# Kernel optimization log

Measured on AMD Instinct MI355X. Metric: run time of the kernel, lower is better.

The kernel has to match this reference:

```python
import jax, jax.numpy as jnp
import numpy as np

D = 1024

def setup_inputs() -> dict:
    key = jax.random.key(0)
    ks = jax.random.split(key, 9)
    B, S = 4, 2048
    s = 1.0 / np.sqrt(D)
    return {
        "query": jax.random.normal(ks[0], (B, S, D), jnp.float32),
        "key": jax.random.normal(ks[1], (B, S, D), jnp.float32),
        "value": jax.random.normal(ks[2], (B, S, D), jnp.float32),
        "Wq": jax.random.normal(ks[3], (D, D), jnp.float32) * s,
        "bq": jax.random.normal(ks[4], (D,), jnp.float32) * 0.01,
        "Wk": jax.random.normal(ks[5], (D, D), jnp.float32) * s,
        "bk": jax.random.normal(ks[6], (D,), jnp.float32) * 0.01,
        "Wv": jax.random.normal(ks[7], (D, D), jnp.float32) * s,
        "bv": jax.random.normal(ks[8], (D,), jnp.float32) * 0.01,
    }

def reference(query, key, value, Wq, bq, Wk, bk, Wv, bv):
    scale = 1.0 / (query.shape[-1] ** 0.5)
    q = jnp.einsum('bsd,ed->bse', query, Wq) + bq  # nn.Linear: x @ W.T + b
    k = jnp.einsum('bsd,ed->bse', key, Wk) + bk
    v = jnp.einsum('bsd,ed->bse', value, Wv) + bv
    scores = jnp.einsum('bqd,bkd->bqk', q, k) * scale  # [B, Sq, Skv]
    w = jax.nn.softmax(scores, axis=-1)
    return jnp.einsum('bqk,bkd->bqd', w, v)
```

## Files before the change

### kernel.cpp

```cpp
#include <hip/hip_runtime.h>

typedef __bf16 bf16x8 __attribute__((ext_vector_type(8)));
typedef float f32x4 __attribute__((ext_vector_type(4)));
typedef unsigned short u16x8 __attribute__((ext_vector_type(8)));

__device__ inline unsigned short f2bf(float f) {
  union { float f; unsigned u; } a; a.f = f;
  return (unsigned short)((a.u + 0x7fffu + ((a.u >> 16) & 1u)) >> 16);
}
__device__ inline float bf2f(unsigned short h) {
  union { unsigned u; float f; } a; a.u = ((unsigned)h) << 16;
  return a.f;
}

__global__ __launch_bounds__(256) void cvtW(const float* __restrict__ Wq,
                                            const float* __restrict__ Wk,
                                            const float* __restrict__ Wv,
                                            unsigned short* __restrict__ Wb) {
  int i = blockIdx.x * 256 + threadIdx.x;
  int idx = i >> 18;
  int off = i & 262143;
  const float* s = (idx == 0) ? Wq : ((idx == 1) ? Wk : Wv);
  float4 v = ((const float4*)s)[off];
  ushort4 o;
  o.x = f2bf(v.x); o.y = f2bf(v.y); o.z = f2bf(v.z); o.w = f2bf(v.w);
  ((ushort4*)(Wb + idx * 1048576))[off] = o;
}

#define G2L(gp, lp) __builtin_amdgcn_global_load_lds( \
    (const __attribute__((address_space(1))) void*)(gp), \
    (__attribute__((address_space(3))) void*)(lp), 16, 0, 0)

#define MFMA_(d, a, b) d = __builtin_amdgcn_mfma_f32_16x16x32_bf16(a, b, d, 0, 0, 0)
#define SB0() __builtin_amdgcn_sched_barrier(0)
#define LGKM(n) do { asm volatile("s_waitcnt lgkmcnt(" #n ")" ::: "memory"); SB0(); } while (0)
#define VMC(n) do { asm volatile("s_waitcnt vmcnt(" #n ")" ::: "memory"); SB0(); } while (0)

struct PJ {
  const float* A0; const float* A1; const float* A2;
  const unsigned short* B;
  unsigned short* outQ; unsigned short* outK; unsigned short* outV;
  const float* biasQ; const float* biasK; const float* biasV;
};

__global__ __launch_bounds__(256) void gemmP(PJ p) {
  extern __shared__ char smem[];
  char* smA = smem;
  char* smB = smem + 32768;
  const int tid = threadIdx.x, lane = tid & 63, wid = tid >> 6;
  const int wm = wid >> 1, wn = wid & 1;

  int orig = blockIdx.x + 8 * (blockIdx.y + 64 * blockIdx.z);
  int wg = (orig & 7) * 192 + (orig >> 3);
  int bx = wg & 7; int t2 = wg >> 3; int by = t2 & 63; int z = t2 >> 6;
  const int m0 = by << 7, n0 = bx << 7;

  const float* Az = (z == 0) ? p.A0 : ((z == 1) ? p.A1 : p.A2);

  const char* srcA0 = (const char*)Az + ((long long)m0 + (tid >> 4)) * 4096
                    + ((tid & 15) << 4);
  const int trow = tid >> 3;
  const int cs = (((tid & 7) ^ (trow & 7)) << 4);
  const char* srcB = (const char*)(p.B + (long long)z * 1048576
                                   + (long long)(n0 + trow) * 1024) + cs;

  const int aRowB = (((wm << 6) + (lane & 15)) << 7);
  const int bRowB = (((wn << 6) + (lane & 15)) << 7);
  const int csw = (lane & 7) << 4;
  const int ck0 = (((lane >> 4) << 4)) ^ csw;
  const int ck1 = ((((lane >> 4) << 4)) | 64) ^ csw;

  f32x4 acc[4][4];
#pragma unroll
  for (int i = 0; i < 4; ++i)
#pragma unroll
    for (int j = 0; j < 4; ++j) acc[i][j] = (f32x4){0.f, 0.f, 0.f, 0.f};

  float4 aregA[8], aregB[8];
  bf16x8 aLo[2][2], aHi[2][2], bLo[2][2], bHi[2][2];

  auto ldA = [&](int t, float4 (&ar)[8]) {
    const char* s = srcA0 + (long long)t * 256;
#pragma unroll
    for (int c = 0; c < 8; ++c)
      ar[c] = *(const float4*)(s + (long long)c * 65536);
  };
  auto wrA = [&](int t, float4 (&ar)[8]) {
    char* dA = smA + ((t & 1) << 14);
    const int g = (tid & 15) >> 1;
    const int hb = (tid & 1) << 3;
#pragma unroll
    for (int c = 0; c < 8; ++c) {
      const int rc = (c << 4) + (tid >> 4);
      float4 v = ar[c];
      union { __bf16 b[4]; ushort4 u; } o;
      o.b[0] = (__bf16)v.x; o.b[1] = (__bf16)v.y;
      o.b[2] = (__bf16)v.z; o.b[3] = (__bf16)v.w;
      *(ushort4*)(dA + (rc << 7) + ((g ^ (rc & 7)) << 4) + hb) = o.u;
    }
  };
  auto stageB = [&](int t, int b) {
    char* dB = smB + (b << 14) + (tid << 4);
    const char* sB = srcB + (long long)t * 128;
#pragma unroll
    for (int c = 0; c < 4; ++c)
      G2L(sB + (long long)c * 65536, dB + (c << 12));
  };
  auto readAh = [&](int b, int half, bf16x8 (&dst)[2][2]) {
    const char* ra = smA + (b << 14) + aRowB + (half << 12);
#pragma unroll
    for (int mi = 0; mi < 2; ++mi) {
      dst[mi][0] = *(const bf16x8*)(ra + (mi << 11) + ck0);
      dst[mi][1] = *(const bf16x8*)(ra + (mi << 11) + ck1);
    }
  };
  auto readBh = [&](int b, int half, bf16x8 (&dst)[2][2]) {
    const char* rb = smB + (b << 14) + bRowB + (half << 12);
#pragma unroll
    for (int ni = 0; ni < 2; ++ni) {
      dst[ni][0] = *(const bf16x8*)(rb + (ni << 11) + ck0);
      dst[ni][1] = *(const bf16x8*)(rb + (ni << 11) + ck1);
    }
  };
  auto quad = [&](int qa, int qb, bf16x8 (&A)[2][2], bf16x8 (&B)[2][2]) {
    __builtin_amdgcn_s_setprio(1);
#pragma unroll
    for (int mi = 0; mi < 2; ++mi)
#pragma unroll
      for (int ni = 0; ni < 2; ++ni) {
        MFMA_(acc[qa * 2 + mi][qb * 2 + ni], A[mi][0], B[ni][0]);
        MFMA_(acc[qa * 2 + mi][qb * 2 + ni], A[mi][1], B[ni][1]);
      }
    __builtin_amdgcn_s_setprio(0);
  };

  const int NT = 16;
  int b0 = 0, b1 = 1, b2 = 2;

  ldA(0, aregA); stageB(0, 0);
  ldA(1, aregB); stageB(1, 1);
  VMC(12);
  wrA(0, aregA);
  LGKM(0);
  __builtin_amdgcn_s_barrier();
  readAh(0, 0, aLo); readBh(0, 0, bLo);
  SB0();

  auto body = [&](int t, float4 (&arW)[8], float4 (&arL)[8]) {
    const bool pf1 = (t + 1) < NT, pf2 = (t + 2) < NT;
    if (pf2) { ldA(t + 2, arL); stageB(t + 2, b2); }
    readAh(t & 1, 1, aHi);
    SB0();
    LGKM(4);
    quad(0, 0, aLo, bLo);
    readBh(b0, 1, bHi);
    SB0();
    LGKM(4);
    quad(1, 0, aHi, bLo);
    LGKM(0);
    quad(0, 1, aLo, bHi);
    quad(1, 1, aHi, bHi);
    if (pf2) { VMC(12); }
    else     { VMC(0);  }
    if (pf1) wrA(t + 1, arW);
    LGKM(0);
    __builtin_amdgcn_s_barrier();
    if (pf1) { readAh((t + 1) & 1, 0, aLo); readBh(b1, 0, bLo); }
    SB0();
    int tmp = b0; b0 = b1; b1 = b2; b2 = tmp;
  };
  for (int t = 0; t < NT; t += 2) { body(t, aregB, aregA); body(t + 1, aregA, aregB); }

  const int c0 = lane & 15, r0 = (lane >> 4) << 2;
  if (z < 2) {
    unsigned short* O = (z == 0) ? p.outQ : p.outK;
    const float* bias = (z == 0) ? p.biasQ : p.biasK;
#pragma unroll
    for (int mi = 0; mi < 4; ++mi) {
      const int grow = m0 + (wm << 6) + (mi << 4) + r0;
#pragma unroll
      for (int ni = 0; ni < 4; ++ni) {
        const int gcol = n0 + (wn << 6) + (ni << 4) + c0;
        const float bb = bias[gcol];
#pragma unroll
        for (int rr = 0; rr < 4; ++rr)
          O[(long long)(grow + rr) * 1024 + gcol] = f2bf(acc[mi][ni][rr] + bb);
      }
    }
  } else {
#pragma unroll
    for (int mi = 0; mi < 4; ++mi) {
      const int grow = m0 + (wm << 6) + (mi << 4) + r0;
      const int bb = grow >> 11, s = grow & 2047;
#pragma unroll
      for (int ni = 0; ni < 4; ++ni) {
        const int d = n0 + (wn << 6) + (ni << 4) + c0;
        const float ba = p.biasV[d];
        ushort4 pk;
        pk.x = f2bf(acc[mi][ni][0] + ba);
        pk.y = f2bf(acc[mi][ni][1] + ba);
        pk.z = f2bf(acc[mi][ni][2] + ba);
        pk.w = f2bf(acc[mi][ni][3] + ba);
        *(ushort4*)(p.outV + ((long long)bb << 21) + (long long)d * 2048 + s) = pk;
      }
    }
  }
}

#define EPI_SCALE 1
#define EPI_OUT 2

struct GP {
  const unsigned short* A;
  const unsigned short* B;
  unsigned short* C;
  long long batchA, batchB, batchC;
  int lda, ldb, ldc, K;
  float scale;
};

template<int BM, int BN, int WMW, int WNW, int EPI>
__global__ __launch_bounds__(512, 2) void gemm2(GP p) {
  constexpr int NWN = BN / WNW;
  constexpr int AMF = WMW / 16, BNF = WNW / 16;
  constexpr int AH = AMF / 2, BH = BNF / 2;
  constexpr int AF_N = AH * 2;
  constexpr int NBA = BM / 64, NBB = BN / 64;
  static_assert((BM / WMW) * NWN == 8, "8 waves");
  static_assert(BNF == 4, "lgkm immediates assume BNF==4");

  extern __shared__ char smem[];
  char* smA = smem;
  char* smB = smem + 2 * BM * 128;

  const int tid = threadIdx.x;
  const int lane = tid & 63;
  const int wid = tid >> 6;
  const int wm = wid / NWN, wn = wid % NWN;

  const int gx = gridDim.x, gy = gridDim.y;
  const int nwg = gx * gy * (int)gridDim.z;
  int orig = blockIdx.x + gx * (blockIdx.y + gy * blockIdx.z);
  int qq = nwg >> 3, rr_ = nwg & 7;
  int xcd = orig & 7, sl = orig >> 3;
  int wg = (xcd < rr_ ? xcd * (qq + 1) : rr_ * (qq + 1) + (xcd - rr_) * qq) + sl;
  int bx = wg % gx;
  int t2 = wg / gx;
  int by = t2 % gy;
  int z  = t2 / gy;

  const int m0 = by * BM, n0 = bx * BN;

  const long long lda2 = (long long)p.lda * 2;
  const long long ldb2 = (long long)p.ldb * 2;
  const char* Abase = (const char*)(p.A + (long long)z * p.batchA) + (long long)m0 * lda2;
  const char* Bbase = (const char*)(p.B + (long long)z * p.batchB) + (long long)n0 * ldb2;

  const int trow = tid >> 3;
  const int cs = (((tid & 7) ^ (trow & 7)) << 4);
  const char* srcA = Abase + (long long)trow * lda2 + cs;
  const char* srcB = Bbase + (long long)trow * ldb2 + cs;

  const int NT = p.K >> 6;

  const int aRowB = ((wm * WMW + (lane & 15)) << 7);
  const int bRowB = ((wn * WNW + (lane & 15)) << 7);
  const int csw = (lane & 7) << 4;
  const int ck0 = (((lane >> 4) << 4)) ^ csw;
  const int ck1 = ((((lane >> 4) << 4)) | 64) ^ csw;

  f32x4 acc[AMF][BNF];
#pragma unroll
  for (int i = 0; i < AMF; ++i)
#pragma unroll
    for (int j = 0; j < BNF; ++j) acc[i][j] = (f32x4){0.f, 0.f, 0.f, 0.f};

  bf16x8 aLo[AH][2], aHi[AH][2], bLo[BH][2], bHi[BH][2];

  auto stage = [&](int t) {
    char* dA = smA + (t & 1) * (BM * 128) + (tid << 4);
    char* dB = smB + (t & 1) * (BN * 128) + (tid << 4);
    const char* sA = srcA + (long long)t * 128;
    const char* sB = srcB + (long long)t * 128;
#pragma unroll
    for (int c = 0; c < NBA; ++c) G2L(sA + (long long)c * (lda2 << 6), dA + c * 8192);
#pragma unroll
    for (int c = 0; c < NBB; ++c) G2L(sB + (long long)c * (ldb2 << 6), dB + c * 8192);
  };
  auto readAh = [&](int t, int half, bf16x8 (&dst)[AH][2]) {
    const char* ra = smA + (t & 1) * (BM * 128) + aRowB + half * (AH * 2048);
#pragma unroll
    for (int mi = 0; mi < AH; ++mi) {
      dst[mi][0] = *(const bf16x8*)(ra + mi * 2048 + ck0);
      dst[mi][1] = *(const bf16x8*)(ra + mi * 2048 + ck1);
    }
  };
  auto readBh = [&](int t, int half, bf16x8 (&dst)[BH][2]) {
    const char* rb = smB + (t & 1) * (BN * 128) + bRowB + half * (BH * 2048);
#pragma unroll
    for (int ni = 0; ni < BH; ++ni) {
      dst[ni][0] = *(const bf16x8*)(rb + ni * 2048 + ck0);
      dst[ni][1] = *(const bf16x8*)(rb + ni * 2048 + ck1);
    }
  };
  auto quad = [&](int qa, int qb, bf16x8 (&A)[AH][2], bf16x8 (&B)[BH][2]) {
    __builtin_amdgcn_s_setprio(1);
#pragma unroll
    for (int mi = 0; mi < AH; ++mi)
#pragma unroll
      for (int ni = 0; ni < BH; ++ni) {
        MFMA_(acc[qa * AH + mi][qb * BH + ni], A[mi][0], B[ni][0]);
        MFMA_(acc[qa * AH + mi][qb * BH + ni], A[mi][1], B[ni][1]);
      }
    __builtin_amdgcn_s_setprio(0);
  };

  stage(0); stage(1);
  if constexpr (NBA + NBB == 8) VMC(8); else VMC(6);
  __builtin_amdgcn_s_barrier();
  readAh(0, 0, aLo); readBh(0, 0, bLo);
  SB0();

  for (int t = 0; t < NT; ++t) {
    readAh(t, 1, aHi);
    SB0();
    if constexpr (AF_N == 8) LGKM(8); else LGKM(4);
    quad(0, 0, aLo, bLo);
    readBh(t, 1, bHi);
    SB0();
    LGKM(4);
    quad(1, 0, aHi, bLo);
    LGKM(0);
    quad(0, 1, aLo, bHi);
    quad(1, 1, aHi, bHi);
    VMC(0);
    __builtin_amdgcn_s_barrier();
    if (t + 2 < NT) stage(t + 2);
    if (t + 1 < NT) { readAh(t + 1, 0, aLo); readBh(t + 1, 0, bLo); }
    SB0();
  }

  const int c0 = lane & 15;
  const int r0 = (lane >> 4) << 2;
  if constexpr (EPI == EPI_SCALE) {
    unsigned short* Cz = p.C + (long long)z * p.batchC;
#pragma unroll
    for (int mi = 0; mi < AMF; ++mi) {
      const int grow = m0 + wm * WMW + (mi << 4) + r0;
#pragma unroll
      for (int ni = 0; ni < BNF; ++ni) {
        const int gcol = n0 + wn * WNW + (ni << 4) + c0;
#pragma unroll
        for (int rr = 0; rr < 4; ++rr)
          Cz[(long long)(grow + rr) * p.ldc + gcol] = f2bf(acc[mi][ni][rr] * p.scale);
      }
    }
  } else {
    float* Cz = (float*)p.C + (long long)z * p.batchC;
#pragma unroll
    for (int mi = 0; mi < AMF; ++mi) {
      const int grow = m0 + wm * WMW + (mi << 4) + r0;
#pragma unroll
      for (int ni = 0; ni < BNF; ++ni) {
        const int gcol = n0 + wn * WNW + (ni << 4) + c0;
#pragma unroll
        for (int rr = 0; rr < 4; ++rr)
          Cz[(long long)(grow + rr) * p.ldc + gcol] = acc[mi][ni][rr] * p.scale;
      }
    }
  }
}

__global__ __launch_bounds__(256) void softmax_rows(unsigned short* __restrict__ S) {
  const size_t row = blockIdx.x;
  unsigned short* pp = S + row * 2048;
  const int t = threadIdx.x, lane = t & 63, wave = t >> 6;
  u16x8 h = ((const u16x8*)pp)[t];
  float x[8];
#pragma unroll
  for (int j = 0; j < 8; ++j) x[j] = bf2f(h[j]);
  float m = x[0];
#pragma unroll
  for (int j = 1; j < 8; ++j) m = fmaxf(m, x[j]);
#pragma unroll
  for (int off = 32; off >= 1; off >>= 1) m = fmaxf(m, __shfl_xor(m, off, 64));
  __shared__ float rmax[4], rsum[4];
  if (lane == 0) rmax[wave] = m;
  __syncthreads();
  m = fmaxf(fmaxf(rmax[0], rmax[1]), fmaxf(rmax[2], rmax[3]));
  float e[8], sum = 0.f;
#pragma unroll
  for (int j = 0; j < 8; ++j) { e[j] = __expf(x[j] - m); sum += e[j]; }
#pragma unroll
  for (int off = 32; off >= 1; off >>= 1) sum += __shfl_xor(sum, off, 64);
  if (lane == 0) rsum[wave] = sum;
  __syncthreads();
  sum = rsum[0] + rsum[1] + rsum[2] + rsum[3];
  const float inv = 1.f / sum;
  u16x8 o;
#pragma unroll
  for (int j = 0; j < 8; ++j) o[j] = f2bf(e[j] * inv);
  ((u16x8*)pp)[t] = o;
}

extern "C" void kernel_launch(void* const* d_in, const int* in_sizes, int n_in,
                              void* d_out, int out_size, void* d_ws, size_t ws_size,
                              hipStream_t stream) {
  const float* q  = (const float*)d_in[0];
  const float* k  = (const float*)d_in[1];
  const float* v  = (const float*)d_in[2];
  const float* Wq = (const float*)d_in[3];
  const float* bq = (const float*)d_in[4];
  const float* Wk = (const float*)d_in[5];
  const float* bk = (const float*)d_in[6];
  const float* Wv = (const float*)d_in[7];
  const float* bv = (const float*)d_in[8];

  unsigned short* S  = (unsigned short*)d_ws;
  unsigned short* Wb = S + 16777216;
  unsigned short* qb = Wb + 3145728;
  unsigned short* kb = qb + 8388608;
  unsigned short* vT = kb + 8388608;

  (void)hipFuncSetAttribute((const void*)gemmP,
      hipFuncAttributeMaxDynamicSharedMemorySize, 81920);
  (void)hipFuncSetAttribute((const void*)gemm2<256,256,128,64,EPI_SCALE>,
      hipFuncAttributeMaxDynamicSharedMemorySize, 131072);
  (void)hipFuncSetAttribute((const void*)gemm2<256,128,64,64,EPI_OUT>,
      hipFuncAttributeMaxDynamicSharedMemorySize, 98304);

  cvtW<<<3072, 256, 0, stream>>>(Wq, Wk, Wv, Wb);

  PJ pj{};
  pj.A0 = q; pj.A1 = k; pj.A2 = v;
  pj.B = Wb;
  pj.outQ = qb; pj.outK = kb; pj.outV = vT;
  pj.biasQ = bq; pj.biasK = bk; pj.biasV = bv;
  gemmP<<<dim3(8, 64, 3), 256, 81920, stream>>>(pj);

  GP gs{};
  gs.A = qb; gs.batchA = 2097152; gs.lda = 1024;
  gs.B = kb; gs.batchB = 2097152; gs.ldb = 1024;
  gs.C = S;  gs.batchC = 4194304; gs.ldc = 2048;
  gs.K = 1024; gs.scale = 0.03125f;
  gemm2<256,256,128,64,EPI_SCALE><<<dim3(8, 8, 4), 512, 131072, stream>>>(gs);

  softmax_rows<<<8192, 256, 0, stream>>>(S);

  GP gv{};
  gv.A = S;  gv.batchA = 4194304; gv.lda = 2048;
  gv.B = vT; gv.batchB = 2097152; gv.ldb = 2048;
  gv.C = (unsigned short*)d_out; gv.batchC = 2097152; gv.ldc = 1024;
  gv.K = 2048; gv.scale = 1.f;
  gemm2<256,128,64,64,EPI_OUT><<<dim3(8, 8, 4), 512, 98304, stream>>>(gv);
}
```

Baseline: 166.9 us.

## Add triple-buffered, XCD-remapped PV GEMM kernel with interleaved LDS reads

Result: no change. 167.3 us (+0.2%).

```diff
diff --git a/kernel.cpp b/kernel.cpp
--- a/kernel.cpp
+++ b/kernel.cpp
@@ -371,6 +371,139 @@
   }
 }
 
+__global__ __launch_bounds__(512) void gemmPV(GP p) {
+  constexpr int ABUF = 256 * 128, BBUF = 128 * 128;
+  extern __shared__ char smem[];
+  char* smA = smem;
+  char* smB = smem + 3 * ABUF;
+
+  const int tid = threadIdx.x;
+  const int lane = tid & 63;
+  const int wid = tid >> 6;
+  const int wm = wid >> 1, wn = wid & 1;
+
+  const int gx = gridDim.x, gy = gridDim.y;
+  const int nwg = gx * gy * (int)gridDim.z;
+  int orig = blockIdx.x + gx * (blockIdx.y + gy * blockIdx.z);
+  int qq = nwg >> 3, rr_ = nwg & 7;
+  int xcd = orig & 7, sl = orig >> 3;
+  int wg = (xcd < rr_ ? xcd * (qq + 1) : rr_ * (qq + 1) + (xcd - rr_) * qq) + sl;
+  int bx = wg % gx;
+  int t2 = wg / gx;
+  int by = t2 % gy;
+  int z  = t2 / gy;
+
+  const int m0 = by * 256, n0 = bx * 128;
+
+  const long long lda2 = (long long)p.lda * 2;
+  const long long ldb2 = (long long)p.ldb * 2;
+  const char* Abase = (const char*)(p.A + (long long)z * p.batchA) + (long long)m0 * lda2;
+  const char* Bbase = (const char*)(p.B + (long long)z * p.batchB) + (long long)n0 * ldb2;
+
+  const int trow = tid >> 3;
+  const int cs = (((tid & 7) ^ (trow & 7)) << 4);
+  const char* srcA = Abase + (long long)trow * lda2 + cs;
+  const char* srcB = Bbase + (long long)trow * ldb2 + cs;
+
+  const int NT = p.K >> 6;
+
+  const int aRowB = ((wm * 64 + (lane & 15)) << 7);
+  const int bRowB = ((wn * 64 + (lane & 15)) << 7);
+  const int csw = (lane & 7) << 4;
+  const int ck0 = (((lane >> 4) << 4)) ^ csw;
+  const int ck1 = ((((lane >> 4) << 4)) | 64) ^ csw;
+
+  f32x4 acc[4][4];
+#pragma unroll
+  for (int i = 0; i < 4; ++i)
+#pragma unroll
+    for (int j = 0; j < 4; ++j) acc[i][j] = (f32x4){0.f, 0.f, 0.f, 0.f};
+
+  bf16x8 aLo[2][2], aHi[2][2], bLo[2][2], bHi[2][2];
+
+  auto stage = [&](int t, int b) {
+    char* dA = smA + b * ABUF + (tid << 4);
+    char* dB = smB + b * BBUF + (tid << 4);
+    const char* sA = srcA + (long long)t * 128;
+    const char* sB = srcB + (long long)t * 128;
+#pragma unroll
+    for (int c = 0; c < 4; ++c) G2L(sA + (long long)c * (lda2 << 6), dA + c * 8192);
+#pragma unroll
+    for (int c = 0; c < 2; ++c) G2L(sB + (long long)c * (ldb2 << 6), dB + c * 8192);
+  };
+  auto readAh = [&](int b, int half, bf16x8 (&dst)[2][2]) {
+    const char* ra = smA + b * ABUF + aRowB + half * 4096;
+#pragma unroll
+    for (int mi = 0; mi < 2; ++mi) {
+      dst[mi][0] = *(const bf16x8*)(ra + mi * 2048 + ck0);
+      dst[mi][1] = *(const bf16x8*)(ra + mi * 2048 + ck1);
+    }
+  };
+  auto readBh = [&](int b, int half, bf16x8 (&dst)[2][2]) {
+    const char* rb = smB + b * BBUF + bRowB + half * 4096;
+#pragma unroll
+    for (int ni = 0; ni < 2; ++ni) {
+      dst[ni][0] = *(const bf16x8*)(rb + ni * 2048 + ck0);
+      dst[ni][1] = *(const bf16x8*)(rb + ni * 2048 + ck1);
+    }
+  };
+  auto quad = [&](int qa, int qb, bf16x8 (&A)[2][2], bf16x8 (&B)[2][2]) {
+    __builtin_amdgcn_s_setprio(1);
+#pragma unroll
+    for (int mi = 0; mi < 2; ++mi)
+#pragma unroll
+      for (int ni = 0; ni < 2; ++ni) {
+        MFMA_(acc[qa * 2 + mi][qb * 2 + ni], A[mi][0], B[ni][0]);
+        MFMA_(acc[qa * 2 + mi][qb * 2 + ni], A[mi][1], B[ni][1]);
+      }
+    __builtin_amdgcn_s_setprio(0);
+  };
+
+  int b0 = 0, b1 = 1, b2 = 2;
+
+  stage(0, 0); stage(1, 1);
+  VMC(6);
+  __builtin_amdgcn_s_barrier();
+  readAh(0, 0, aLo); readBh(0, 0, bLo);
+  SB0();
+
+  for (int t = 0; t < NT; ++t) {
+    if (t + 2 < NT) stage(t + 2, b2);
+    readAh(b0, 1, aHi);
+    SB0();
+    LGKM(4);
+    quad(0, 0, aLo, bLo);
+    readBh(b0, 1, bHi);
+    SB0();
+    LGKM(4);
+    quad(1, 0, aHi, bLo);
+    LGKM(0);
+    quad(0, 1, aLo, bHi);
+    quad(1, 1, aHi, bHi);
+    if (t + 2 < NT) { VMC(6); }
+    else            { VMC(0); }
+    __builtin_amdgcn_s_barrier();
+    if (t + 1 < NT) { readAh(b1, 0, aLo); readBh(b1, 0, bLo); }
+    SB0();
+    int tmp = b0; b0 = b1; b1 = b2; b2 = tmp;
+  }
+
+  const int c0 = lane & 15;
+  const int r0 = (lane >> 4) << 2;
+  float* Cz = (float*)p.C + (long long)z * p.batchC;
+#pragma unroll
+  for (int mi = 0; mi < 4; ++mi) {
+    const int grow = m0 + wm * 64 + (mi << 4) + r0;
+#pragma unroll
+    for (int ni = 0; ni < 4; ++ni) {
+      const int gcol = n0 + wn * 64 + (ni << 4) + c0;
+#pragma unroll
+      for (int rr = 0; rr < 4; ++rr)
+        Cz[(long long)(grow + rr) * p.ldc + gcol] = acc[mi][ni][rr] * p.scale;
+    }
+  }
+}
+
 __global__ __launch_bounds__(256) void softmax_rows(unsigned short* __restrict__ S) {
   const size_t row = blockIdx.x;
   unsigned short* pp = S + row * 2048;
@@ -426,8 +559,8 @@
       hipFuncAttributeMaxDynamicSharedMemorySize, 81920);
   (void)hipFuncSetAttribute((const void*)gemm2<256,256,128,64,EPI_SCALE>,
       hipFuncAttributeMaxDynamicSharedMemorySize, 131072);
-  (void)hipFuncSetAttribute((const void*)gemm2<256,128,64,64,EPI_OUT>,
-      hipFuncAttributeMaxDynamicSharedMemorySize, 98304);
+  (void)hipFuncSetAttribute((const void*)gemmPV,
+      hipFuncAttributeMaxDynamicSharedMemorySize, 147456);
 
   cvtW<<<3072, 256, 0, stream>>>(Wq, Wk, Wv, Wb);
 
@@ -452,5 +585,5 @@
   gv.B = vT; gv.batchB = 2097152; gv.ldb = 2048;
   gv.C = (unsigned short*)d_out; gv.batchC = 2097152; gv.ldc = 1024;
   gv.K = 2048; gv.scale = 1.f;
-  gemm2<256,128,64,64,EPI_OUT><<<dim3(8, 8, 4), 512, 98304, stream>>>(gv);
-}
+  gemmPV<<<dim3(8, 8, 4), 512, 147456, stream>>>(gv);
+}
```
